# Kernel optimization log

Hardware: AMD Instinct MI355X
Metric: run time of the kernel (lower is better)

## Reference

```python
import jax, jax.numpy as jnp
import numpy as np

H = 4096
DFF = 16384
EPS = 1e-5

def _layernorm(x, gamma, beta, eps):
    mu = jnp.mean(x, axis=-1, keepdims=True)
    var = jnp.var(x, axis=-1, keepdims=True)
    return (x - mu) * jax.lax.rsqrt(var + eps) * gamma + beta

def setup_inputs() -> dict:
    key = jax.random.key(0)
    ks = jax.random.split(key, 9)
    B, S = 2, 2048
    s_h = 1.0 / np.sqrt(H)
    s_f = 1.0 / np.sqrt(DFF)
    return {
        "input": jax.random.normal(ks[0], (B, S, H), jnp.float32),
        "residual": jax.random.normal(ks[1], (B, S, H), jnp.float32),
        "residual_norm": jax.random.normal(ks[2], (B, S, H), jnp.float32),
        "bias": jax.random.normal(ks[3], (H,), jnp.float32) * 0.02,
        "attn_nw": 1.0 + jax.random.normal(ks[4], (H,), jnp.float32) * 0.02,
        "attn_nb": jax.random.normal(ks[5], (H,), jnp.float32) * 0.02,
        "inter_w": jax.random.normal(ks[6], (H, DFF), jnp.float32) * s_h,
        "inter_b": jax.random.normal(ks[7], (DFF,), jnp.float32) * 0.02,
        "output_w": jax.random.normal(ks[8], (DFF, H), jnp.float32) * s_f,
        "output_b": jnp.zeros((H,), jnp.float32),
    }

def reference(input, residual, residual_norm, bias, attn_nw, attn_nb,
              inter_w, inter_b, output_w, output_b):
    # mlp_gemm (pre_layer_norm, mlp_after_attn, fp32, no quant):
    # LN(input + residual + attn_bias) -> GEMM -> GeLU -> GEMM
    ln_in = input + residual + bias                      # [B,S,H]
    ln = _layernorm(ln_in, attn_nw, attn_nb, EPS)        # [B,S,H]
    inter = jax.nn.gelu(jnp.einsum('bsh,hf->bsf', ln, inter_w) + inter_b,
                        approximate=True)                # [B,S,DFF]
    out = jnp.einsum('bsf,fh->bsh', inter, output_w)     # [B,S,H]
    # residual_add (preln, add_bias, mp_size=1):
    # residual = mlp_out + residual + attn_out + (attn_bias + mlp_bias)/mp_size
    return out + residual + input + (bias + output_b)
```

## Files before the change

kernel.cpp:

```cpp
#include <hip/hip_runtime.h>
#include <cstdint>
#include <cstddef>

#define H_DIM 4096
#define DFF_DIM 16384
#define NROWS 4096

typedef unsigned short bf16_t;
typedef __attribute__((ext_vector_type(8))) short bf16x8;
typedef __attribute__((ext_vector_type(4))) float f32x4;
typedef __attribute__((ext_vector_type(4))) unsigned short u16x4;

static __device__ __forceinline__ bf16_t f2bf(float f) {
  union { float f; unsigned int i; } v; v.f = f;
  unsigned int x = v.i;
  return (bf16_t)((x + 0x7fffu + ((x >> 16) & 1u)) >> 16);
}

#define GLDS16(gp, lp)                                                    \
  __builtin_amdgcn_global_load_lds(                                       \
      (__attribute__((address_space(1))) void*)(gp),                      \
      (__attribute__((address_space(3))) void*)(lp), 16, 0, 0)

#define SB0 __builtin_amdgcn_sched_barrier(0)

__global__ __launch_bounds__(256) void fused_ln_kernel(
    const float* __restrict__ inp, const float* __restrict__ res,
    const float* __restrict__ bias, const float* __restrict__ gamma,
    const float* __restrict__ beta, bf16_t* __restrict__ out) {
  int row = blockIdx.x;
  int t = threadIdx.x;
  const float4* pin = (const float4*)(inp + (size_t)row * H_DIM);
  const float4* pre = (const float4*)(res + (size_t)row * H_DIM);
  const float4* pbi = (const float4*)bias;
  float4 xv[4];
  float s = 0.f, ss = 0.f;
#pragma unroll
  for (int i = 0; i < 4; ++i) {
    int idx = t + i * 256;
    float4 a = pin[idx];
    float4 b = pre[idx];
    float4 c = pbi[idx];
    float4 v;
    v.x = a.x + b.x + c.x;
    v.y = a.y + b.y + c.y;
    v.z = a.z + b.z + c.z;
    v.w = a.w + b.w + c.w;
    xv[i] = v;
    s += v.x + v.y + v.z + v.w;
    ss += v.x * v.x + v.y * v.y + v.z * v.z + v.w * v.w;
  }
#pragma unroll
  for (int off = 32; off > 0; off >>= 1) {
    s += __shfl_xor(s, off);
    ss += __shfl_xor(ss, off);
  }
  __shared__ float sred[8];
  int w = t >> 6, l = t & 63;
  if (l == 0) { sred[w] = s; sred[4 + w] = ss; }
  __syncthreads();
  s = sred[0] + sred[1] + sred[2] + sred[3];
  ss = sred[4] + sred[5] + sred[6] + sred[7];
  const float inv = 1.f / (float)H_DIM;
  float mean = s * inv;
  float var = ss * inv - mean * mean;
  float rstd = rsqrtf(var + 1e-5f);
  const float4* pg = (const float4*)gamma;
  const float4* pb = (const float4*)beta;
#pragma unroll
  for (int i = 0; i < 4; ++i) {
    int idx = t + i * 256;
    float4 g = pg[idx];
    float4 bb = pb[idx];
    float4 v = xv[i];
    u16x4 o;
    o.x = f2bf((v.x - mean) * rstd * g.x + bb.x);
    o.y = f2bf((v.y - mean) * rstd * g.y + bb.y);
    o.z = f2bf((v.z - mean) * rstd * g.z + bb.z);
    o.w = f2bf((v.w - mean) * rstd * g.w + bb.w);
    *(u16x4*)(out + (size_t)row * H_DIM + (size_t)idx * 4) = o;
  }
}

__global__ __launch_bounds__(256) void transpose_cvt_kernel(
    const float* __restrict__ W, bf16_t* __restrict__ Wt, int K, int N) {
  __shared__ float tile[64][65];
  int nb = N >> 6;
  int bk = blockIdx.x / nb;
  int bn = blockIdx.x - bk * nb;
  int t = threadIdx.x;
  int r = t >> 4;
  int c4 = (t & 15) << 2;
#pragma unroll
  for (int p = 0; p < 4; ++p) {
    int row = r + p * 16;
    float4 v = *(const float4*)(W + (size_t)(bk * 64 + row) * N + bn * 64 + c4);
    tile[row][c4 + 0] = v.x;
    tile[row][c4 + 1] = v.y;
    tile[row][c4 + 2] = v.z;
    tile[row][c4 + 3] = v.w;
  }
  __syncthreads();
#pragma unroll
  for (int p = 0; p < 4; ++p) {
    int nn = r + p * 16;
    u16x4 o;
    o.x = f2bf(tile[c4 + 0][nn]);
    o.y = f2bf(tile[c4 + 1][nn]);
    o.z = f2bf(tile[c4 + 2][nn]);
    o.w = f2bf(tile[c4 + 3][nn]);
    *(u16x4*)(Wt + (size_t)(bn * 64 + nn) * K + bk * 64 + c4) = o;
  }
}

#define PHASE_MFMA(MIBASE)                                                  \
  __builtin_amdgcn_s_setprio(1);                                            \
  _Pragma("unroll") for (int ii = 0; ii < 4; ++ii)                          \
      _Pragma("unroll") for (int jj = 0; jj < 4; ++jj) acc[MIBASE + ii][jj] = \
      __builtin_amdgcn_mfma_f32_16x16x32_bf16(aF[ii], bF[jj],               \
                                              acc[MIBASE + ii][jj], 0, 0, 0); \
  __builtin_amdgcn_s_setprio(0);

template <int EPI>
__global__ __launch_bounds__(512, 2) void gemm8p_kernel(
    const bf16_t* __restrict__ A, const bf16_t* __restrict__ Bt,
    int M, int N, int K,
    const float* __restrict__ eb1, const float* __restrict__ eb2,
    const float* __restrict__ add1, const float* __restrict__ add2,
    bf16_t* __restrict__ outb, float* __restrict__ outf) {
  __shared__ char lds[163840];

  const int t = threadIdx.x;
  const int l = t & 63;
  const int wid = t >> 6;
  const int wr = wid >> 2;
  const int wc = wid & 3;

  int nwg = gridDim.x;
  int bid = blockIdx.x;
  int wg = (bid & 7) * (nwg >> 3) + (bid >> 3);
  int ntm = M >> 8;
  int chunk = wg >> 5, s5 = wg & 31;
  int cmn = ntm >> 3;
  int cm = chunk % cmn, cn = chunk / cmn;
  int tm = cm * 8 + (s5 & 7);
  int tn = cn * 4 + (s5 >> 3);
  size_t m0 = (size_t)tm * 256, n0 = (size_t)tn * 256;

  f32x4 acc[8][4];
#pragma unroll
  for (int i = 0; i < 8; ++i)
#pragma unroll
    for (int j = 0; j < 4; ++j) acc[i][j] = {0.f, 0.f, 0.f, 0.f};

  const int c0 = t, c1 = t + 512;
  const int row0 = c0 >> 2, row1 = c1 >> 2;
  const int ks0 = (c0 & 3) ^ ((row0 >> 1) & 3);
  const int ks1 = (c1 & 3) ^ ((row1 >> 1) & 3);
  const bf16_t* pA0 = A + (m0 + row0) * (size_t)K + ks0 * 8;
  const bf16_t* pA1 = A + (m0 + row1) * (size_t)K + ks1 * 8;
  const bf16_t* pB0 = Bt + (n0 + row0) * (size_t)K + ks0 * 8;
  const bf16_t* pB1 = Bt + (n0 + row1) * (size_t)K + ks1 * 8;

  auto stageA = [&](int base, int h, int T) {
    GLDS16(pA0 + (size_t)T * 64 + h * 32, lds + base + h * 16384 + c0 * 16);
    GLDS16(pA1 + (size_t)T * 64 + h * 32, lds + base + h * 16384 + c1 * 16);
  };
  auto stageB = [&](int base, int h, int T) {
    GLDS16(pB0 + (size_t)T * 64 + h * 32, lds + base + h * 16384 + c0 * 16);
    GLDS16(pB1 + (size_t)T * 64 + h * 32, lds + base + h * 16384 + c1 * 16);
  };

  const int slot = (((l >> 4) ^ ((l >> 1) & 3)) << 4);
  int aoffs[8], boffs[4];
#pragma unroll
  for (int mi = 0; mi < 8; ++mi)
    aoffs[mi] = (wr * 128 + mi * 16 + (l & 15)) * 64 + slot;
#pragma unroll
  for (int nj = 0; nj < 4; ++nj)
    boffs[nj] = (wc * 64 + nj * 16 + (l & 15)) * 64 + slot;

  auto rd8 = [&](int off) -> bf16x8 {
    return *(const bf16x8*)(const void*)(lds + off);
  };

  const int NT = K >> 6;

  stageA(0, 0, 0);
  stageB(98304, 0, 0);
  stageA(0, 1, 0);
  stageB(98304, 1, 0);
  stageA(32768, 0, 1);
  stageB(98304 + 32768, 0, 1);
  stageA(32768, 1, 1);
  stageB(98304 + 32768, 1, 1);
  SB0;
  asm volatile("s_waitcnt vmcnt(8)" ::: "memory");
  SB0;
  __builtin_amdgcn_s_barrier();

  int aC = 0, aS = 2;
  for (int T = 0; T < NT; ++T) {
    const int bB = 98304 + (T & 1) * 32768;
    const int aCb = aC * 32768;
    const int aSb = aS * 32768;
    int Tg = T + 2;
    if (Tg >= NT) Tg = NT - 1;
    bf16x8 aF[4], bF[4];
#pragma unroll
    for (int j = 0; j < 4; ++j) bF[j] = rd8(bB + boffs[j]);
#pragma unroll
    for (int i2 = 0; i2 < 4; ++i2) aF[i2] = rd8(aCb + aoffs[i2]);
    stageA(aSb, 0, Tg);
    PHASE_MFMA(0)
    __builtin_amdgcn_s_barrier();
#pragma unroll
    for (int i2 = 0; i2 < 4; ++i2) aF[i2] = rd8(aCb + aoffs[4 + i2]);
    stageB(bB, 0, Tg);
    PHASE_MFMA(4)
    __builtin_amdgcn_s_barrier();
#pragma unroll
    for (int j = 0; j < 4; ++j) bF[j] = rd8(bB + boffs[j] + 16384);
#pragma unroll
    for (int i2 = 0; i2 < 4; ++i2) aF[i2] = rd8(aCb + aoffs[i2] + 16384);
    stageA(aSb, 1, Tg);
    PHASE_MFMA(0)
    __builtin_amdgcn_s_barrier();
#pragma unroll
    for (int i2 = 0; i2 < 4; ++i2) aF[i2] = rd8(aCb + aoffs[4 + i2] + 16384);
    stageB(bB, 1, Tg);
    PHASE_MFMA(4)
    SB0;
    asm volatile("s_waitcnt vmcnt(8)" ::: "memory");
    SB0;
    __builtin_amdgcn_s_barrier();
    aS = aC;
    aC = (aC == 2) ? 0 : aC + 1;
  }
  asm volatile("s_waitcnt vmcnt(0)" ::: "memory");

  int mb = (int)m0 + wr * 128;
  int nb2 = (int)n0 + wc * 64;
  int lr = (l >> 4) * 4;
  int lc = l & 15;
#pragma unroll
  for (int mi = 0; mi < 8; ++mi) {
#pragma unroll
    for (int i2 = 0; i2 < 4; ++i2) {
      int rrow = mb + mi * 16 + lr + i2;
      size_t base = (size_t)rrow * N;
#pragma unroll
      for (int nj = 0; nj < 4; ++nj) {
        int col = nb2 + nj * 16 + lc;
        float v = acc[mi][nj][i2];
        if (EPI == 0) {
          float x = v + eb1[col];
          float u = 0.7978845608028654f * (x + 0.044715f * x * x * x);
          float th = 1.f - 2.f / (__expf(2.f * u) + 1.f);
          outb[base + col] = f2bf(0.5f * x * (1.f + th));
        } else {
          outf[base + col] =
              v + eb1[col] + eb2[col] + add1[base + col] + add2[base + col];
        }
      }
    }
  }
}

extern "C" void kernel_launch(void* const* d_in, const int* in_sizes, int n_in,
                              void* d_out, int out_size, void* d_ws,
                              size_t ws_size, hipStream_t stream) {
  const float* input = (const float*)d_in[0];
  const float* residual = (const float*)d_in[1];
  const float* bias = (const float*)d_in[3];
  const float* attn_nw = (const float*)d_in[4];
  const float* attn_nb = (const float*)d_in[5];
  const float* inter_w = (const float*)d_in[6];
  const float* inter_b = (const float*)d_in[7];
  const float* output_w = (const float*)d_in[8];
  const float* output_b = (const float*)d_in[9];
  float* out = (float*)d_out;

  char* ws = (char*)d_ws;
  bf16_t* lnb = (bf16_t*)ws;
  bf16_t* w1t = (bf16_t*)(ws + (size_t)NROWS * H_DIM * 2);
  bf16_t* w2t = (bf16_t*)(ws + (size_t)NROWS * H_DIM * 2 +
                          (size_t)H_DIM * DFF_DIM * 2);
  bf16_t* inter = (bf16_t*)(ws + (size_t)NROWS * H_DIM * 2 +
                            2 * (size_t)H_DIM * DFF_DIM * 2);

  fused_ln_kernel<<<NROWS, 256, 0, stream>>>(input, residual, bias, attn_nw,
                                             attn_nb, lnb);
  transpose_cvt_kernel<<<(H_DIM / 64) * (DFF_DIM / 64), 256, 0, stream>>>(
      inter_w, w1t, H_DIM, DFF_DIM);
  transpose_cvt_kernel<<<(DFF_DIM / 64) * (H_DIM / 64), 256, 0, stream>>>(
      output_w, w2t, DFF_DIM, H_DIM);
  gemm8p_kernel<0><<<(NROWS / 256) * (DFF_DIM / 256), 512, 0, stream>>>(
      lnb, w1t, NROWS, DFF_DIM, H_DIM, inter_b, nullptr, nullptr, nullptr,
      inter, nullptr);
  gemm8p_kernel<1><<<(NROWS / 256) * (H_DIM / 256), 512, 0, stream>>>(
      inter, w2t, NROWS, H_DIM, DFF_DIM, bias, output_b, residual, input,
      nullptr, out);
}
```

Before: 1.198 ms.

## Software-pipeline LDS fragment reads one phase ahead of MFMA in GEMM loop

Measured after the change: 1.192 ms. Within noise of the previous version (-0.5%).

```diff
diff --git a/kernel.cpp b/kernel.cpp
--- a/kernel.cpp
+++ b/kernel.cpp
@@ -113,11 +113,11 @@
   }
 }
 
-#define PHASE_MFMA(MIBASE)                                                  \
+#define MFMA16(AB, BB, MIBASE)                                              \
   __builtin_amdgcn_s_setprio(1);                                            \
   _Pragma("unroll") for (int ii = 0; ii < 4; ++ii)                          \
       _Pragma("unroll") for (int jj = 0; jj < 4; ++jj) acc[MIBASE + ii][jj] = \
-      __builtin_amdgcn_mfma_f32_16x16x32_bf16(aF[ii], bF[jj],               \
+      __builtin_amdgcn_mfma_f32_16x16x32_bf16(AB[ii], BB[jj],               \
                                               acc[MIBASE + ii][jj], 0, 0, 0); \
   __builtin_amdgcn_s_setprio(0);
 
@@ -199,41 +199,60 @@
   SB0;
   __builtin_amdgcn_s_barrier();
 
+  bf16x8 bP[4], aL[4], aH[4], bQ[4], aL2[4], aH2[4];
+#pragma unroll
+  for (int j = 0; j < 4; ++j) bP[j] = rd8(98304 + boffs[j]);
+#pragma unroll
+  for (int i = 0; i < 4; ++i) aL[i] = rd8(aoffs[i]);
+
   int aC = 0, aS = 2;
   for (int T = 0; T < NT; ++T) {
     const int bB = 98304 + (T & 1) * 32768;
+    const int bBn = 98304 + ((T + 1) & 1) * 32768;
     const int aCb = aC * 32768;
+    const int aCn = (aC == 2 ? 0 : aC + 1) * 32768;
     const int aSb = aS * 32768;
     int Tg = T + 2;
     if (Tg >= NT) Tg = NT - 1;
-    bf16x8 aF[4], bF[4];
-#pragma unroll
-    for (int j = 0; j < 4; ++j) bF[j] = rd8(bB + boffs[j]);
-#pragma unroll
-    for (int i2 = 0; i2 < 4; ++i2) aF[i2] = rd8(aCb + aoffs[i2]);
+
+#pragma unroll
+    for (int i2 = 0; i2 < 4; ++i2) aH[i2] = rd8(aCb + aoffs[4 + i2]);
     stageA(aSb, 0, Tg);
-    PHASE_MFMA(0)
+    SB0;
+    MFMA16(aL, bP, 0)
+    asm volatile("s_waitcnt lgkmcnt(0)" ::: "memory");
     __builtin_amdgcn_s_barrier();
-#pragma unroll
-    for (int i2 = 0; i2 < 4; ++i2) aF[i2] = rd8(aCb + aoffs[4 + i2]);
+
+#pragma unroll
+    for (int j = 0; j < 4; ++j) bQ[j] = rd8(bB + boffs[j] + 16384);
+#pragma unroll
+    for (int i2 = 0; i2 < 4; ++i2) aL2[i2] = rd8(aCb + aoffs[i2] + 16384);
     stageB(bB, 0, Tg);
-    PHASE_MFMA(4)
+    SB0;
+    MFMA16(aH, bP, 4)
+    asm volatile("s_waitcnt lgkmcnt(0)" ::: "memory");
     __builtin_amdgcn_s_barrier();
-#pragma unroll
-    for (int j = 0; j < 4; ++j) bF[j] = rd8(bB + boffs[j] + 16384);
-#pragma unroll
-    for (int i2 = 0; i2 < 4; ++i2) aF[i2] = rd8(aCb + aoffs[i2] + 16384);
+
+#pragma unroll
+    for (int i2 = 0; i2 < 4; ++i2) aH2[i2] = rd8(aCb + aoffs[4 + i2] + 16384);
     stageA(aSb, 1, Tg);
-    PHASE_MFMA(0)
+    SB0;
+    MFMA16(aL2, bQ, 0)
+    SB0;
+    asm volatile("s_waitcnt vmcnt(6) lgkmcnt(0)" ::: "memory");
+    SB0;
     __builtin_amdgcn_s_barrier();
-#pragma unroll
-    for (int i2 = 0; i2 < 4; ++i2) aF[i2] = rd8(aCb + aoffs[4 + i2] + 16384);
+
+#pragma unroll
+    for (int j = 0; j < 4; ++j) bP[j] = rd8(bBn + boffs[j]);
+#pragma unroll
+    for (int i2 = 0; i2 < 4; ++i2) aL[i2] = rd8(aCn + aoffs[i2]);
     stageB(bB, 1, Tg);
-    PHASE_MFMA(4)
-    SB0;
-    asm volatile("s_waitcnt vmcnt(8)" ::: "memory");
-    SB0;
+    SB0;
+    MFMA16(aH2, bQ, 4)
+    asm volatile("s_waitcnt lgkmcnt(0)" ::: "memory");
     __builtin_amdgcn_s_barrier();
+
     aS = aC;
     aC = (aC == 2) ? 0 : aC + 1;
   }
```

## Restructure GEMM main loop into double-buffered 64-wide K tiles with quadrant MFMA phases

Applied to the files above, without the earlier changes.

Result: faster. 1.068 ms (-10.8%).

```diff
diff --git a/kernel.cpp b/kernel.cpp
--- a/kernel.cpp
+++ b/kernel.cpp
@@ -113,13 +113,19 @@
   }
 }
 
-#define PHASE_MFMA(MIBASE)                                                  \
+#define QMFMA(AQ, BQ, MILO, NJLO)                                           \
   __builtin_amdgcn_s_setprio(1);                                            \
-  _Pragma("unroll") for (int ii = 0; ii < 4; ++ii)                          \
-      _Pragma("unroll") for (int jj = 0; jj < 4; ++jj) acc[MIBASE + ii][jj] = \
-      __builtin_amdgcn_mfma_f32_16x16x32_bf16(aF[ii], bF[jj],               \
-                                              acc[MIBASE + ii][jj], 0, 0, 0); \
+  _Pragma("unroll") for (int i5 = 0; i5 < 4; ++i5)                          \
+  _Pragma("unroll") for (int j5 = 0; j5 < 2; ++j5)                          \
+  _Pragma("unroll") for (int k5 = 0; k5 < 2; ++k5)                          \
+    acc[MILO + i5][NJLO + j5] = __builtin_amdgcn_mfma_f32_16x16x32_bf16(    \
+        AQ[i5 * 2 + k5], BQ[j5 * 2 + k5], acc[MILO + i5][NJLO + j5], 0, 0, 0); \
   __builtin_amdgcn_s_setprio(0);
+
+#define BAR __builtin_amdgcn_s_barrier()
+#define LGKM0 do { asm volatile("s_waitcnt lgkmcnt(0)" ::: "memory"); SB0; } while (0)
+#define LGKM8 do { asm volatile("s_waitcnt lgkmcnt(8)" ::: "memory"); } while (0)
+#define VM6 do { SB0; asm volatile("s_waitcnt vmcnt(6)" ::: "memory"); SB0; } while (0)
 
 template <int EPI>
 __global__ __launch_bounds__(512, 2) void gemm8p_kernel(
@@ -128,7 +134,7 @@
     const float* __restrict__ eb1, const float* __restrict__ eb2,
     const float* __restrict__ add1, const float* __restrict__ add2,
     bf16_t* __restrict__ outb, float* __restrict__ outf) {
-  __shared__ char lds[163840];
+  __shared__ char lds[131072];
 
   const int t = threadIdx.x;
   const int l = t & 63;
@@ -153,105 +159,150 @@
 #pragma unroll
     for (int j = 0; j < 4; ++j) acc[i][j] = {0.f, 0.f, 0.f, 0.f};
 
-  const int c0 = t, c1 = t + 512;
-  const int row0 = c0 >> 2, row1 = c1 >> 2;
-  const int ks0 = (c0 & 3) ^ ((row0 >> 1) & 3);
-  const int ks1 = (c1 & 3) ^ ((row1 >> 1) & 3);
-  const bf16_t* pA0 = A + (m0 + row0) * (size_t)K + ks0 * 8;
-  const bf16_t* pA1 = A + (m0 + row1) * (size_t)K + ks1 * 8;
-  const bf16_t* pB0 = Bt + (n0 + row0) * (size_t)K + ks0 * 8;
-  const bf16_t* pB1 = Bt + (n0 + row1) * (size_t)K + ks1 * 8;
-
-  auto stageA = [&](int base, int h, int T) {
-    GLDS16(pA0 + (size_t)T * 64 + h * 32, lds + base + h * 16384 + c0 * 16);
-    GLDS16(pA1 + (size_t)T * 64 + h * 32, lds + base + h * 16384 + c1 * 16);
+  const int rh = t >> 3;
+  const int sl = t & 7;
+  const int oc = sl ^ ((rh >> 1) & 7);
+  const bf16_t* sA0 = A + (m0 + rh) * (size_t)K + oc * 8;
+  const bf16_t* sA1 = A + (m0 + rh + 64) * (size_t)K + oc * 8;
+  const bf16_t* sB0 = Bt + (n0 + rh) * (size_t)K + oc * 8;
+  const bf16_t* sB1 = Bt + (n0 + rh + 64) * (size_t)K + oc * 8;
+
+  auto stA = [&](int b, int h, int T) {
+    GLDS16(sA0 + (size_t)h * 128 * K + (size_t)T * 64,
+           lds + b * 32768 + h * 16384 + t * 16);
+    GLDS16(sA1 + (size_t)h * 128 * K + (size_t)T * 64,
+           lds + b * 32768 + h * 16384 + (t + 512) * 16);
   };
-  auto stageB = [&](int base, int h, int T) {
-    GLDS16(pB0 + (size_t)T * 64 + h * 32, lds + base + h * 16384 + c0 * 16);
-    GLDS16(pB1 + (size_t)T * 64 + h * 32, lds + base + h * 16384 + c1 * 16);
+  auto stB = [&](int b, int h, int T) {
+    GLDS16(sB0 + (size_t)h * 128 * K + (size_t)T * 64,
+           lds + 65536 + b * 32768 + h * 16384 + t * 16);
+    GLDS16(sB1 + (size_t)h * 128 * K + (size_t)T * 64,
+           lds + 65536 + b * 32768 + h * 16384 + (t + 512) * 16);
   };
 
-  const int slot = (((l >> 4) ^ ((l >> 1) & 3)) << 4);
-  int aoffs[8], boffs[4];
-#pragma unroll
-  for (int mi = 0; mi < 8; ++mi)
-    aoffs[mi] = (wr * 128 + mi * 16 + (l & 15)) * 64 + slot;
-#pragma unroll
-  for (int nj = 0; nj < 4; ++nj)
-    boffs[nj] = (wc * 64 + nj * 16 + (l & 15)) * 64 + slot;
+  int offA[8][2], offB[4][2];
+#pragma unroll
+  for (int mi = 0; mi < 8; ++mi) {
+    int h = mi >> 2;
+    int lr = (mi & 3) * 32 + wr * 16 + (l & 15);
+#pragma unroll
+    for (int ks = 0; ks < 2; ++ks) {
+      int o = ks * 4 + (l >> 4);
+      offA[mi][ks] = h * 16384 + lr * 128 + ((o ^ ((lr >> 1) & 7)) << 4);
+    }
+  }
+#pragma unroll
+  for (int nj = 0; nj < 4; ++nj) {
+    int h = nj >> 1;
+    int lc = (nj & 1) * 64 + wc * 16 + (l & 15);
+#pragma unroll
+    for (int ks = 0; ks < 2; ++ks) {
+      int o = ks * 4 + (l >> 4);
+      offB[nj][ks] = 65536 + h * 16384 + lc * 128 + ((o ^ ((lc >> 1) & 7)) << 4);
+    }
+  }
 
   auto rd8 = [&](int off) -> bf16x8 {
     return *(const bf16x8*)(const void*)(lds + off);
   };
 
   const int NT = K >> 6;
-
-  stageA(0, 0, 0);
-  stageB(98304, 0, 0);
-  stageA(0, 1, 0);
-  stageB(98304, 1, 0);
-  stageA(32768, 0, 1);
-  stageB(98304 + 32768, 0, 1);
-  stageA(32768, 1, 1);
-  stageB(98304 + 32768, 1, 1);
+  const int NI = NT >> 1;
+
+  stB(0, 0, 0); stA(0, 0, 0); stB(0, 1, 0); stA(0, 1, 0);
+  stB(1, 0, 1); stA(1, 0, 1); stB(1, 1, 1);
   SB0;
-  asm volatile("s_waitcnt vmcnt(8)" ::: "memory");
+  asm volatile("s_waitcnt vmcnt(6)" ::: "memory");
   SB0;
-  __builtin_amdgcn_s_barrier();
-
-  int aC = 0, aS = 2;
-  for (int T = 0; T < NT; ++T) {
-    const int bB = 98304 + (T & 1) * 32768;
-    const int aCb = aC * 32768;
-    const int aSb = aS * 32768;
-    int Tg = T + 2;
-    if (Tg >= NT) Tg = NT - 1;
-    bf16x8 aF[4], bF[4];
-#pragma unroll
-    for (int j = 0; j < 4; ++j) bF[j] = rd8(bB + boffs[j]);
-#pragma unroll
-    for (int i2 = 0; i2 < 4; ++i2) aF[i2] = rd8(aCb + aoffs[i2]);
-    stageA(aSb, 0, Tg);
-    PHASE_MFMA(0)
-    __builtin_amdgcn_s_barrier();
-#pragma unroll
-    for (int i2 = 0; i2 < 4; ++i2) aF[i2] = rd8(aCb + aoffs[4 + i2]);
-    stageB(bB, 0, Tg);
-    PHASE_MFMA(4)
-    __builtin_amdgcn_s_barrier();
-#pragma unroll
-    for (int j = 0; j < 4; ++j) bF[j] = rd8(bB + boffs[j] + 16384);
-#pragma unroll
-    for (int i2 = 0; i2 < 4; ++i2) aF[i2] = rd8(aCb + aoffs[i2] + 16384);
-    stageA(aSb, 1, Tg);
-    PHASE_MFMA(0)
-    __builtin_amdgcn_s_barrier();
-#pragma unroll
-    for (int i2 = 0; i2 < 4; ++i2) aF[i2] = rd8(aCb + aoffs[4 + i2] + 16384);
-    stageB(bB, 1, Tg);
-    PHASE_MFMA(4)
-    SB0;
-    asm volatile("s_waitcnt vmcnt(8)" ::: "memory");
-    SB0;
-    __builtin_amdgcn_s_barrier();
-    aS = aC;
-    aC = (aC == 2) ? 0 : aC + 1;
+  BAR;
+
+  bf16x8 aQ[8], bQ0[4], bQ1[4];
+  for (int it = 0; it < NI; ++it) {
+    const int Tb = 2 * it + 1;
+    int Sa = 2 * it + 2; if (Sa >= NT) Sa = NT - 1;
+    int Sb = 2 * it + 3; if (Sb >= NT) Sb = NT - 1;
+
+#pragma unroll
+    for (int i = 0; i < 4; ++i)
+#pragma unroll
+      for (int ks = 0; ks < 2; ++ks) aQ[i * 2 + ks] = rd8(offA[i][ks]);
+#pragma unroll
+    for (int j = 0; j < 2; ++j)
+#pragma unroll
+      for (int ks = 0; ks < 2; ++ks) bQ0[j * 2 + ks] = rd8(offB[j][ks]);
+    stA(1, 1, Tb);
+    SB0; LGKM8; BAR; LGKM0;
+    QMFMA(aQ, bQ0, 0, 0)
+    BAR;
+#pragma unroll
+    for (int j = 0; j < 2; ++j)
+#pragma unroll
+      for (int ks = 0; ks < 2; ++ks) bQ1[j * 2 + ks] = rd8(offB[2 + j][ks]);
+    stB(0, 0, Sa);
+    SB0; BAR; LGKM0;
+    QMFMA(aQ, bQ1, 0, 2)
+    BAR;
+#pragma unroll
+    for (int i = 0; i < 4; ++i)
+#pragma unroll
+      for (int ks = 0; ks < 2; ++ks) aQ[i * 2 + ks] = rd8(offA[4 + i][ks]);
+    stA(0, 0, Sa);
+    SB0; BAR; LGKM0;
+    QMFMA(aQ, bQ1, 4, 2)
+    BAR;
+    stB(0, 1, Sa);
+    VM6; BAR;
+    QMFMA(aQ, bQ0, 4, 0)
+    BAR;
+
+#pragma unroll
+    for (int i = 0; i < 4; ++i)
+#pragma unroll
+      for (int ks = 0; ks < 2; ++ks) aQ[i * 2 + ks] = rd8(32768 + offA[i][ks]);
+#pragma unroll
+    for (int j = 0; j < 2; ++j)
+#pragma unroll
+      for (int ks = 0; ks < 2; ++ks) bQ0[j * 2 + ks] = rd8(32768 + offB[j][ks]);
+    stA(0, 1, Sa);
+    SB0; LGKM8; BAR; LGKM0;
+    QMFMA(aQ, bQ0, 0, 0)
+    BAR;
+#pragma unroll
+    for (int j = 0; j < 2; ++j)
+#pragma unroll
+      for (int ks = 0; ks < 2; ++ks)
+        bQ1[j * 2 + ks] = rd8(32768 + offB[2 + j][ks]);
+    stB(1, 0, Sb);
+    SB0; BAR; LGKM0;
+    QMFMA(aQ, bQ1, 0, 2)
+    BAR;
+#pragma unroll
+    for (int i = 0; i < 4; ++i)
+#pragma unroll
+      for (int ks = 0; ks < 2; ++ks)
+        aQ[i * 2 + ks] = rd8(32768 + offA[4 + i][ks]);
+    stA(1, 0, Sb);
+    SB0; BAR; LGKM0;
+    QMFMA(aQ, bQ1, 4, 2)
+    BAR;
+    stB(1, 1, Sb);
+    VM6; BAR;
+    QMFMA(aQ, bQ0, 4, 0)
+    BAR;
   }
   asm volatile("s_waitcnt vmcnt(0)" ::: "memory");
 
-  int mb = (int)m0 + wr * 128;
-  int nb2 = (int)n0 + wc * 64;
-  int lr = (l >> 4) * 4;
+  int lr4 = (l >> 4) * 4;
   int lc = l & 15;
 #pragma unroll
   for (int mi = 0; mi < 8; ++mi) {
 #pragma unroll
     for (int i2 = 0; i2 < 4; ++i2) {
-      int rrow = mb + mi * 16 + lr + i2;
+      int rrow = (int)m0 + (mi * 2 + wr) * 16 + lr4 + i2;
       size_t base = (size_t)rrow * N;
 #pragma unroll
       for (int nj = 0; nj < 4; ++nj) {
-        int col = nb2 + nj * 16 + lc;
+        int col = (int)n0 + (nj * 4 + wc) * 16 + lc;
         float v = acc[mi][nj][i2];
         if (EPI == 0) {
           float x = v + eb1[col];
```
